# Optimization experiments

Hardware: AMD Instinct MI355X
Metric: run time of the kernel (lower is better)

The kernel has to match this reference:

```python
import jax, jax.numpy as jnp
import numpy as np

N = 50000      # nodes
E = 800000     # edges (avg degree 16)
D = 128        # in_channels == hidden_channels (required by x*M + x_hat*~M)
OUT = 64       # fc out_channels


def _linear_params(key, out_f, in_f):
    # torch.nn.Linear default init: U(-1/sqrt(in), 1/sqrt(in))
    bound = 1.0 / np.sqrt(in_f)
    kw, kb = jax.random.split(key)
    W = jax.random.uniform(kw, (out_f, in_f), jnp.float32, -bound, bound)
    b = jax.random.uniform(kb, (out_f,), jnp.float32, -bound, bound)
    return W, b


def setup_inputs() -> dict:
    key = jax.random.key(0)
    ks = jax.random.split(key, 8)
    x = jax.random.normal(ks[0], (N, D), jnp.float32)
    edge_index = jax.random.randint(ks[1], (2, E), 0, N, dtype=jnp.int64)
    edge_weight = jax.random.uniform(ks[2], (E,), jnp.float32)
    M = jax.random.randint(ks[3], (N, D), 0, 2) > 0  # bool mask
    W1, b1 = _linear_params(ks[4], D, D)
    W2, b2 = _linear_params(ks[5], D, D)
    W3, b3 = _linear_params(ks[6], D, D)
    Wf, bf = _linear_params(ks[7], OUT, D)
    # extra Parameter `bias` in each FPLayer is zero-initialized
    z = jnp.zeros((D,), jnp.float32)
    return {"edge_index": edge_index, "edge_weight": edge_weight, "x": x, "M": M,
            "W1": W1, "b1": b1, "bias1": z, "W2": W2, "b2": b2, "bias2": z,
            "W3": W3, "b3": b3, "bias3": z, "Wf": Wf, "bf": bf}


def reference(edge_index, edge_weight, x, M,
              W1, b1, bias1, W2, b2, bias2, W3, b3, bias3, Wf, bf):
    row, col = edge_index[0], edge_index[1]
    n = x.shape[0]
    # symmetric degree normalization based on destination-node in-degree
    deg = jax.ops.segment_sum(jnp.ones(row.shape[0], x.dtype), col, num_segments=n)
    safe = jnp.where(deg > 0, deg, 1.0)
    dinv = jnp.where(deg > 0, 1.0 / jnp.sqrt(safe), 0.0)
    norm = dinv[row] * dinv[col]  # [E]  (edge_weight is unused by message())

    def fp_layer(x_tilde, W, b, bias):
        msg = norm[:, None] * x_tilde[row]                      # [E, D] gather
        agg = jax.ops.segment_sum(msg, col, num_segments=n)     # [N, D] scatter-add
        return agg @ W.T + b + bias

    # conv1: x_hat = 0 -> x_tilde = x*M
    h = jax.nn.relu(fp_layer(jnp.where(M, x, 0.0), W1, b1, bias1))
    h = jax.nn.relu(fp_layer(jnp.where(M, x, h), W2, b2, bias2))
    h = jax.nn.relu(fp_layer(jnp.where(M, x, h), W3, b3, bias3))
    return h @ Wf.T + bf
```

## Files before the change

### kernel.cpp

```cpp
#include <hip/hip_runtime.h>

#define DD 128
#define OUTF 64
#define SCAP 128

typedef __attribute__((ext_vector_type(8))) _Float16 fp16x8;
typedef __attribute__((ext_vector_type(8))) unsigned short ushort8;
typedef __attribute__((ext_vector_type(4))) float floatx4;

union h16 { _Float16 f; unsigned short u; };

__global__ void probe_kernel(const unsigned char* m8, const int* ei32, int* flags) {
    __shared__ int s_u8, s_not64;
    int t = threadIdx.x;
    if (t == 0) { s_u8 = 0; s_not64 = 0; }
    __syncthreads();
    for (int i = t; i < 4096; i += 256)
        if ((i & 3) && m8[i]) s_u8 = 1;
    for (int i = t; i < 1024; i += 256)
        if (ei32[2 * i + 1]) s_not64 = 1;
    __syncthreads();
    if (t == 0) { flags[0] = s_u8; flags[1] = s_not64 ? 0 : 1; }
}

__global__ __launch_bounds__(256) void setup_kernel(
    const int* ei, const int* flags, int* cursor, int* __restrict__ slot, int E, int n,
    const float* __restrict__ x, const void* __restrict__ M,
    _Float16* __restrict__ xsel, int nd4,
    const float* __restrict__ W1, const float* __restrict__ W2,
    const float* __restrict__ W3, const float* __restrict__ Wf,
    _Float16* __restrict__ Bh1, _Float16* __restrict__ Bl1,
    _Float16* __restrict__ Bh2, _Float16* __restrict__ Bl2,
    _Float16* __restrict__ Bh3, _Float16* __restrict__ Bl3,
    _Float16* __restrict__ Bhf, _Float16* __restrict__ Blf,
    int nbSlot, int nbXt) {
    int bid = blockIdx.x;
    if (bid < nbSlot) {
        int e = bid * 256 + threadIdx.x;
        if (e >= E) return;
        int r, c;
        if (flags[1]) {
            const long long* p = (const long long*)ei;
            r = (int)p[e];
            c = (int)p[(size_t)E + e];
        } else {
            r = ei[e];
            c = ei[E + e];
        }
        r = min(max(r, 0), n - 1);
        c = min(max(c, 0), n - 1);
        int pos = atomicAdd(&cursor[c], 1);
        if (pos < SCAP)
            slot[(size_t)c * SCAP + pos] = r;
    } else if (bid < nbSlot + nbXt) {
        int i4 = (bid - nbSlot) * 256 + threadIdx.x;
        if (i4 >= nd4) return;
        size_t base = (size_t)i4 * 4;
        const float4 xv = *(const float4*)&x[base];
        int m0, m1, m2, m3;
        if (flags[0]) {
            const unsigned char* mp = (const unsigned char*)M + base;
            m0 = mp[0]; m1 = mp[1]; m2 = mp[2]; m3 = mp[3];
        } else {
            const int* mp = (const int*)M + base;
            m0 = mp[0]; m1 = mp[1]; m2 = mp[2]; m3 = mp[3];
        }
        h16 h0, h1, h2, h3;
        h0.f = (_Float16)xv.x; h1.f = (_Float16)xv.y;
        h2.f = (_Float16)xv.z; h3.f = (_Float16)xv.w;
        unsigned short s0 = m0 ? h0.u : (unsigned short)0xFFFF;
        unsigned short s1 = m1 ? h1.u : (unsigned short)0xFFFF;
        unsigned short s2 = m2 ? h2.u : (unsigned short)0xFFFF;
        unsigned short s3 = m3 ? h3.u : (unsigned short)0xFFFF;
        unsigned long long pk = (unsigned long long)s0 | ((unsigned long long)s1 << 16)
                              | ((unsigned long long)s2 << 32) | ((unsigned long long)s3 << 48);
        *(unsigned long long*)&xsel[base] = pk;
    } else {
        int tid = (bid - nbSlot - nbXt) * 256 + threadIdx.x;
        const float* W; _Float16 *Bh, *Bl; int NT, lt;
        if      (tid < 2048) { W = W1; Bh = Bh1; Bl = Bl1; NT = 8; lt = tid; }
        else if (tid < 4096) { W = W2; Bh = Bh2; Bl = Bl2; NT = 8; lt = tid - 2048; }
        else if (tid < 6144) { W = W3; Bh = Bh3; Bl = Bl3; NT = 8; lt = tid - 4096; }
        else if (tid < 7168) { W = Wf; Bh = Bhf; Bl = Blf; NT = 4; lt = tid - 6144; }
        else return;
        int lane = lt & 63;
        int g = lt >> 6;
        int nt = g % NT;
        int chunk = g / NT;
        int o = nt * 16 + (lane & 15);
        int k = chunk * 32 + (lane >> 4) * 8;
        const float* src = W + o * 128 + k;
#pragma unroll
        for (int j = 0; j < 8; j++) {
            float a = src[j];
            _Float16 h = (_Float16)a;
            Bh[(size_t)lt * 8 + j] = h;
            Bl[(size_t)lt * 8 + j] = (_Float16)(a - (float)h);
        }
    }
}

template <int MODE>
__global__ __launch_bounds__(256) void layer_kernel(
    const _Float16* __restrict__ xin,
    const int* __restrict__ cursor,
    const int* __restrict__ slot,
    const _Float16* __restrict__ Bh,
    const _Float16* __restrict__ Bl,
    const float* __restrict__ b,
    const float* __restrict__ bias,
    const _Float16* __restrict__ B2h,
    const _Float16* __restrict__ B2l,
    const float* __restrict__ b2,
    float* __restrict__ out_f,
    const _Float16* __restrict__ xsel,
    _Float16* __restrict__ xt_out,
    int n) {
    __shared__ __align__(16) _Float16 sh[4][16][136];
    int wid = (blockIdx.x * 256 + threadIdx.x) >> 6;
    int nwaves = n >> 4;
    if (wid >= nwaves) return;
    int n0 = wid * 16;
    int lane = threadIdx.x & 63;
    int li = lane & 15;
    int quad = lane >> 4;
    int wv = (threadIdx.x >> 6) & 3;

    for (int m = 0; m < 16; m++) {
        int node = n0 + m;
        int craw = cursor[node];
        int cnt = min(craw, SCAP);
        float dc = craw > 0 ? rsqrtf((float)craw) : 0.0f;
        const int* sl = slot + (size_t)node * SCAP;
        float acc[8] = {0.f, 0.f, 0.f, 0.f, 0.f, 0.f, 0.f, 0.f};
        for (int k = 0; k < cnt; k += 16) {
            int i0 = k + quad;
            int i1 = k + 4 + quad;
            int i2 = k + 8 + quad;
            int i3 = k + 12 + quad;
            int r0 = sl[min(i0, cnt - 1)];
            int r1 = sl[min(i1, cnt - 1)];
            int r2 = sl[min(i2, cnt - 1)];
            int r3 = sl[min(i3, cnt - 1)];
            int c0 = cursor[r0], c1 = cursor[r1], c2 = cursor[r2], c3 = cursor[r3];
            float w0 = (i0 < cnt && c0 > 0) ? dc * rsqrtf((float)c0) : 0.0f;
            float w1 = (i1 < cnt && c1 > 0) ? dc * rsqrtf((float)c1) : 0.0f;
            float w2 = (i2 < cnt && c2 > 0) ? dc * rsqrtf((float)c2) : 0.0f;
            float w3 = (i3 < cnt && c3 > 0) ? dc * rsqrtf((float)c3) : 0.0f;
            ushort8 u0 = *(const ushort8*)&xin[(size_t)r0 * DD + li * 8];
            ushort8 u1 = *(const ushort8*)&xin[(size_t)r1 * DD + li * 8];
            ushort8 u2 = *(const ushort8*)&xin[(size_t)r2 * DD + li * 8];
            ushort8 u3 = *(const ushort8*)&xin[(size_t)r3 * DD + li * 8];
#pragma unroll
            for (int j = 0; j < 8; j++) {
                h16 t0, t1, t2, t3;
                t0.u = (u0[j] == (unsigned short)0xFFFF) ? (unsigned short)0 : u0[j];
                t1.u = (u1[j] == (unsigned short)0xFFFF) ? (unsigned short)0 : u1[j];
                t2.u = (u2[j] == (unsigned short)0xFFFF) ? (unsigned short)0 : u2[j];
                t3.u = (u3[j] == (unsigned short)0xFFFF) ? (unsigned short)0 : u3[j];
                acc[j] += w0 * (float)t0.f + w1 * (float)t1.f
                        + w2 * (float)t2.f + w3 * (float)t3.f;
            }
        }
#pragma unroll
        for (int j = 0; j < 8; j++) {
            acc[j] += __shfl_xor(acc[j], 16);
            acc[j] += __shfl_xor(acc[j], 32);
        }
        if (quad == 0) {
            fp16x8 o;
#pragma unroll
            for (int j = 0; j < 8; j++) o[j] = (_Float16)acc[j];
            *(fp16x8*)&sh[wv][m][li * 8] = o;
        }
    }
    __asm__ volatile("s_waitcnt lgkmcnt(0)" ::: "memory");

    floatx4 acc[8];
#pragma unroll
    for (int nt = 0; nt < 8; nt++)
        acc[nt] = (floatx4){0.f, 0.f, 0.f, 0.f};
#pragma unroll
    for (int chunk = 0; chunk < 4; chunk++) {
        fp16x8 a = *(const fp16x8*)&sh[wv][li][chunk * 32 + quad * 8];
#pragma unroll
        for (int nt = 0; nt < 8; nt++) {
            size_t boff = (size_t)(((chunk * 8 + nt) << 6) + lane) * 8;
            fp16x8 b_h = *(const fp16x8*)&Bh[boff];
            fp16x8 b_l = *(const fp16x8*)&Bl[boff];
            acc[nt] = __builtin_amdgcn_mfma_f32_16x16x32_f16(a, b_h, acc[nt], 0, 0, 0);
            acc[nt] = __builtin_amdgcn_mfma_f32_16x16x32_f16(a, b_l, acc[nt], 0, 0, 0);
        }
    }
    __asm__ volatile("s_waitcnt lgkmcnt(0)" ::: "memory");

#pragma unroll
    for (int nt = 0; nt < 8; nt++) {
        int o = nt * 16 + li;
        float bb = b[o] + bias[o];
#pragma unroll
        for (int reg = 0; reg < 4; reg++) {
            float v = fmaxf(acc[nt][reg] + bb, 0.0f);
            sh[wv][quad * 4 + reg][o] = (_Float16)v;
        }
    }
    __asm__ volatile("s_waitcnt lgkmcnt(0)" ::: "memory");

    if (MODE == 0) {
#pragma unroll
        for (int it = 0; it < 4; it++) {
            int node = it * 4 + quad;
            size_t ix = (size_t)(n0 + node) * DD + li * 8;
            fp16x8 hv = *(const fp16x8*)&sh[wv][node][li * 8];
            fp16x8 xv = *(const fp16x8*)&xsel[ix];
            ushort8 xb = *(const ushort8*)&xsel[ix];
            fp16x8 o;
#pragma unroll
            for (int j = 0; j < 8; j++)
                o[j] = (xb[j] == (unsigned short)0xFFFF) ? hv[j] : xv[j];
            *(fp16x8*)&xt_out[ix] = o;
        }
    } else {
        floatx4 acc2[4];
#pragma unroll
        for (int nt = 0; nt < 4; nt++)
            acc2[nt] = (floatx4){0.f, 0.f, 0.f, 0.f};
#pragma unroll
        for (int chunk = 0; chunk < 4; chunk++) {
            fp16x8 a2 = *(const fp16x8*)&sh[wv][li][chunk * 32 + quad * 8];
#pragma unroll
            for (int nt = 0; nt < 4; nt++) {
                size_t boff = (size_t)(((chunk * 4 + nt) << 6) + lane) * 8;
                fp16x8 b_h = *(const fp16x8*)&B2h[boff];
                fp16x8 b_l = *(const fp16x8*)&B2l[boff];
                acc2[nt] = __builtin_amdgcn_mfma_f32_16x16x32_f16(a2, b_h, acc2[nt], 0, 0, 0);
                acc2[nt] = __builtin_amdgcn_mfma_f32_16x16x32_f16(a2, b_l, acc2[nt], 0, 0, 0);
            }
        }
        __asm__ volatile("s_waitcnt lgkmcnt(0)" ::: "memory");
        float* shf = (float*)&sh[wv][0][0];
#pragma unroll
        for (int nt = 0; nt < 4; nt++) {
            int o = nt * 16 + li;
            float bb = b2[o];
#pragma unroll
            for (int reg = 0; reg < 4; reg++)
                shf[(quad * 4 + reg) * 68 + o] = acc2[nt][reg] + bb;
        }
        __asm__ volatile("s_waitcnt lgkmcnt(0)" ::: "memory");
#pragma unroll
        for (int it = 0; it < 4; it++) {
            int node = it * 4 + quad;
            float4 v = *(const float4*)&shf[node * 68 + li * 4];
            *(float4*)&out_f[(size_t)(n0 + node) * OUTF + li * 4] = v;
        }
    }
}

extern "C" void kernel_launch(void* const* d_in, const int* in_sizes, int n_in,
                              void* d_out, int out_size, void* d_ws, size_t ws_size,
                              hipStream_t stream) {
    const int*   ei    = (const int*)d_in[0];
    const float* x     = (const float*)d_in[2];
    const void*  M     = d_in[3];
    const float* W1    = (const float*)d_in[4];
    const float* b1    = (const float*)d_in[5];
    const float* bias1 = (const float*)d_in[6];
    const float* W2    = (const float*)d_in[7];
    const float* b2    = (const float*)d_in[8];
    const float* bias2 = (const float*)d_in[9];
    const float* W3    = (const float*)d_in[10];
    const float* b3    = (const float*)d_in[11];
    const float* bias3 = (const float*)d_in[12];
    const float* Wf    = (const float*)d_in[13];
    const float* bf    = (const float*)d_in[14];

    const int E = in_sizes[1];
    const int N = in_sizes[2] / DD;
    const int ND = N * DD;

    char* w = (char*)d_ws;
    size_t off = 0;
    auto alloc = [&](size_t bytes) -> char* {
        char* p = w + off;
        off = (off + bytes + 255) & ~(size_t)255;
        return p;
    };
    int*   flags  = (int*)  alloc(32);
    int*   cursor = (int*)  alloc((size_t)N * 4);
    int*   slot   = (int*)  alloc((size_t)N * SCAP * 4);
    _Float16* xsel = (_Float16*)alloc((size_t)ND * 2);
    _Float16* xt   = (_Float16*)alloc((size_t)ND * 2);
    _Float16* Bh1 = (_Float16*)alloc(128 * 128 * 2);
    _Float16* Bl1 = (_Float16*)alloc(128 * 128 * 2);
    _Float16* Bh2 = (_Float16*)alloc(128 * 128 * 2);
    _Float16* Bl2 = (_Float16*)alloc(128 * 128 * 2);
    _Float16* Bh3 = (_Float16*)alloc(128 * 128 * 2);
    _Float16* Bl3 = (_Float16*)alloc(128 * 128 * 2);
    _Float16* Bhf = (_Float16*)alloc(64 * 128 * 2);
    _Float16* Blf = (_Float16*)alloc(64 * 128 * 2);
    (void)ws_size;

    const int nd4 = ND / 4;
    const int nbSlot = (E + 255) / 256;
    const int nbXt   = (nd4 + 255) / 256;
    const int nbPk   = 28;

    probe_kernel<<<1, 256, 0, stream>>>((const unsigned char*)M, ei, flags);
    hipMemsetAsync(cursor, 0, (size_t)N * 4, stream);
    setup_kernel<<<nbSlot + nbXt + nbPk, 256, 0, stream>>>(
        ei, flags, cursor, slot, E, N,
        x, M, xsel, nd4,
        W1, W2, W3, Wf,
        Bh1, Bl1, Bh2, Bl2, Bh3, Bl3, Bhf, Blf,
        nbSlot, nbXt);

    int nwaves = N / 16;
    int gGrid = (nwaves * 64 + 255) / 256;

    layer_kernel<0><<<gGrid, 256, 0, stream>>>(xsel, cursor, slot, Bh1, Bl1, b1, bias1,
                                               nullptr, nullptr, nullptr, nullptr,
                                               xsel, xt, N);
    layer_kernel<0><<<gGrid, 256, 0, stream>>>(xt, cursor, slot, Bh2, Bl2, b2, bias2,
                                               nullptr, nullptr, nullptr, nullptr,
                                               xsel, xt, N);
    layer_kernel<1><<<gGrid, 256, 0, stream>>>(xt, cursor, slot, Bh3, Bl3, b3, bias3,
                                               Bhf, Blf, bf, (float*)d_out,
                                               nullptr, nullptr, N);
}
```

Measured before the change: 346.8 us.

## Split fused gather-aggregate and MFMA GEMM into separate per-node agg and GEMM kernels

```diff
diff --git a/kernel.cpp b/kernel.cpp
--- a/kernel.cpp
+++ b/kernel.cpp
@@ -100,22 +100,80 @@
     }
 }
 
+template <int SENT>
+__global__ __launch_bounds__(256) void agg_kernel(const _Float16* __restrict__ xin,
+                                                  const int* __restrict__ cursor,
+                                                  const int* __restrict__ slot,
+                                                  _Float16* __restrict__ A, int n) {
+    int wave = (blockIdx.x * 256 + threadIdx.x) >> 6;
+    if (wave >= n) return;
+    int lane = threadIdx.x & 63;
+    int sid = lane >> 4;
+    int li = lane & 15;
+    int craw = cursor[wave];
+    int cnt = min(craw, SCAP);
+    float dc = craw > 0 ? rsqrtf((float)craw) : 0.0f;
+    const int* sl = slot + (size_t)wave * SCAP;
+    float acc[8] = {0.f, 0.f, 0.f, 0.f, 0.f, 0.f, 0.f, 0.f};
+    for (int k = 0; k < cnt; k += 16) {
+        int i0 = k + sid;
+        int i1 = k + 4 + sid;
+        int i2 = k + 8 + sid;
+        int i3 = k + 12 + sid;
+        int r0 = sl[min(i0, cnt - 1)];
+        int r1 = sl[min(i1, cnt - 1)];
+        int r2 = sl[min(i2, cnt - 1)];
+        int r3 = sl[min(i3, cnt - 1)];
+        int c0 = cursor[r0], c1 = cursor[r1], c2 = cursor[r2], c3 = cursor[r3];
+        float w0 = (i0 < cnt && c0 > 0) ? dc * rsqrtf((float)c0) : 0.0f;
+        float w1 = (i1 < cnt && c1 > 0) ? dc * rsqrtf((float)c1) : 0.0f;
+        float w2 = (i2 < cnt && c2 > 0) ? dc * rsqrtf((float)c2) : 0.0f;
+        float w3 = (i3 < cnt && c3 > 0) ? dc * rsqrtf((float)c3) : 0.0f;
+        ushort8 u0 = *(const ushort8*)&xin[(size_t)r0 * DD + li * 8];
+        ushort8 u1 = *(const ushort8*)&xin[(size_t)r1 * DD + li * 8];
+        ushort8 u2 = *(const ushort8*)&xin[(size_t)r2 * DD + li * 8];
+        ushort8 u3 = *(const ushort8*)&xin[(size_t)r3 * DD + li * 8];
+#pragma unroll
+        for (int j = 0; j < 8; j++) {
+            h16 t0, t1, t2, t3;
+            if (SENT) {
+                t0.u = (u0[j] == (unsigned short)0xFFFF) ? (unsigned short)0 : u0[j];
+                t1.u = (u1[j] == (unsigned short)0xFFFF) ? (unsigned short)0 : u1[j];
+                t2.u = (u2[j] == (unsigned short)0xFFFF) ? (unsigned short)0 : u2[j];
+                t3.u = (u3[j] == (unsigned short)0xFFFF) ? (unsigned short)0 : u3[j];
+            } else {
+                t0.u = u0[j]; t1.u = u1[j]; t2.u = u2[j]; t3.u = u3[j];
+            }
+            acc[j] += w0 * (float)t0.f + w1 * (float)t1.f
+                    + w2 * (float)t2.f + w3 * (float)t3.f;
+        }
+    }
+#pragma unroll
+    for (int j = 0; j < 8; j++) {
+        acc[j] += __shfl_xor(acc[j], 16);
+        acc[j] += __shfl_xor(acc[j], 32);
+    }
+    if (sid == 0) {
+        fp16x8 o;
+#pragma unroll
+        for (int j = 0; j < 8; j++) o[j] = (_Float16)acc[j];
+        *(fp16x8*)&A[(size_t)wave * DD + li * 8] = o;
+    }
+}
+
 template <int MODE>
-__global__ __launch_bounds__(256) void layer_kernel(
-    const _Float16* __restrict__ xin,
-    const int* __restrict__ cursor,
-    const int* __restrict__ slot,
-    const _Float16* __restrict__ Bh,
-    const _Float16* __restrict__ Bl,
-    const float* __restrict__ b,
-    const float* __restrict__ bias,
-    const _Float16* __restrict__ B2h,
-    const _Float16* __restrict__ B2l,
-    const float* __restrict__ b2,
-    float* __restrict__ out_f,
-    const _Float16* __restrict__ xsel,
-    _Float16* __restrict__ xt_out,
-    int n) {
+__global__ __launch_bounds__(256) void gemm_mfma(const _Float16* __restrict__ A,
+                                                 const _Float16* __restrict__ Bh,
+                                                 const _Float16* __restrict__ Bl,
+                                                 const float* __restrict__ b,
+                                                 const float* __restrict__ bias,
+                                                 const _Float16* __restrict__ B2h,
+                                                 const _Float16* __restrict__ B2l,
+                                                 const float* __restrict__ b2,
+                                                 float* __restrict__ out_f,
+                                                 const _Float16* __restrict__ xsel,
+                                                 _Float16* __restrict__ xt_out,
+                                                 int n) {
     __shared__ __align__(16) _Float16 sh[4][16][136];
     int wid = (blockIdx.x * 256 + threadIdx.x) >> 6;
     int nwaves = n >> 4;
@@ -126,63 +184,15 @@
     int quad = lane >> 4;
     int wv = (threadIdx.x >> 6) & 3;
 
-    for (int m = 0; m < 16; m++) {
-        int node = n0 + m;
-        int craw = cursor[node];
-        int cnt = min(craw, SCAP);
-        float dc = craw > 0 ? rsqrtf((float)craw) : 0.0f;
-        const int* sl = slot + (size_t)node * SCAP;
-        float acc[8] = {0.f, 0.f, 0.f, 0.f, 0.f, 0.f, 0.f, 0.f};
-        for (int k = 0; k < cnt; k += 16) {
-            int i0 = k + quad;
-            int i1 = k + 4 + quad;
-            int i2 = k + 8 + quad;
-            int i3 = k + 12 + quad;
-            int r0 = sl[min(i0, cnt - 1)];
-            int r1 = sl[min(i1, cnt - 1)];
-            int r2 = sl[min(i2, cnt - 1)];
-            int r3 = sl[min(i3, cnt - 1)];
-            int c0 = cursor[r0], c1 = cursor[r1], c2 = cursor[r2], c3 = cursor[r3];
-            float w0 = (i0 < cnt && c0 > 0) ? dc * rsqrtf((float)c0) : 0.0f;
-            float w1 = (i1 < cnt && c1 > 0) ? dc * rsqrtf((float)c1) : 0.0f;
-            float w2 = (i2 < cnt && c2 > 0) ? dc * rsqrtf((float)c2) : 0.0f;
-            float w3 = (i3 < cnt && c3 > 0) ? dc * rsqrtf((float)c3) : 0.0f;
-            ushort8 u0 = *(const ushort8*)&xin[(size_t)r0 * DD + li * 8];
-            ushort8 u1 = *(const ushort8*)&xin[(size_t)r1 * DD + li * 8];
-            ushort8 u2 = *(const ushort8*)&xin[(size_t)r2 * DD + li * 8];
-            ushort8 u3 = *(const ushort8*)&xin[(size_t)r3 * DD + li * 8];
-#pragma unroll
-            for (int j = 0; j < 8; j++) {
-                h16 t0, t1, t2, t3;
-                t0.u = (u0[j] == (unsigned short)0xFFFF) ? (unsigned short)0 : u0[j];
-                t1.u = (u1[j] == (unsigned short)0xFFFF) ? (unsigned short)0 : u1[j];
-                t2.u = (u2[j] == (unsigned short)0xFFFF) ? (unsigned short)0 : u2[j];
-                t3.u = (u3[j] == (unsigned short)0xFFFF) ? (unsigned short)0 : u3[j];
-                acc[j] += w0 * (float)t0.f + w1 * (float)t1.f
-                        + w2 * (float)t2.f + w3 * (float)t3.f;
-            }
-        }
-#pragma unroll
-        for (int j = 0; j < 8; j++) {
-            acc[j] += __shfl_xor(acc[j], 16);
-            acc[j] += __shfl_xor(acc[j], 32);
-        }
-        if (quad == 0) {
-            fp16x8 o;
-#pragma unroll
-            for (int j = 0; j < 8; j++) o[j] = (_Float16)acc[j];
-            *(fp16x8*)&sh[wv][m][li * 8] = o;
-        }
-    }
-    __asm__ volatile("s_waitcnt lgkmcnt(0)" ::: "memory");
-
     floatx4 acc[8];
 #pragma unroll
     for (int nt = 0; nt < 8; nt++)
         acc[nt] = (floatx4){0.f, 0.f, 0.f, 0.f};
+
+    const _Float16* arow = A + (size_t)(n0 + li) * DD + quad * 8;
 #pragma unroll
     for (int chunk = 0; chunk < 4; chunk++) {
-        fp16x8 a = *(const fp16x8*)&sh[wv][li][chunk * 32 + quad * 8];
+        fp16x8 a = *(const fp16x8*)(arow + chunk * 32);
 #pragma unroll
         for (int nt = 0; nt < 8; nt++) {
             size_t boff = (size_t)(((chunk * 8 + nt) << 6) + lane) * 8;
@@ -192,7 +202,6 @@
             acc[nt] = __builtin_amdgcn_mfma_f32_16x16x32_f16(a, b_l, acc[nt], 0, 0, 0);
         }
     }
-    __asm__ volatile("s_waitcnt lgkmcnt(0)" ::: "memory");
 
 #pragma unroll
     for (int nt = 0; nt < 8; nt++) {
@@ -291,6 +300,7 @@
     int*   slot   = (int*)  alloc((size_t)N * SCAP * 4);
     _Float16* xsel = (_Float16*)alloc((size_t)ND * 2);
     _Float16* xt   = (_Float16*)alloc((size_t)ND * 2);
+    _Float16* Aa   = (_Float16*)alloc((size_t)ND * 2);
     _Float16* Bh1 = (_Float16*)alloc(128 * 128 * 2);
     _Float16* Bl1 = (_Float16*)alloc(128 * 128 * 2);
     _Float16* Bh2 = (_Float16*)alloc(128 * 128 * 2);
@@ -317,14 +327,18 @@
 
     int nwaves = N / 16;
     int gGrid = (nwaves * 64 + 255) / 256;
-
-    layer_kernel<0><<<gGrid, 256, 0, stream>>>(xsel, cursor, slot, Bh1, Bl1, b1, bias1,
-                                               nullptr, nullptr, nullptr, nullptr,
-                                               xsel, xt, N);
-    layer_kernel<0><<<gGrid, 256, 0, stream>>>(xt, cursor, slot, Bh2, Bl2, b2, bias2,
-                                               nullptr, nullptr, nullptr, nullptr,
-                                               xsel, xt, N);
-    layer_kernel<1><<<gGrid, 256, 0, stream>>>(xt, cursor, slot, Bh3, Bl3, b3, bias3,
-                                               Bhf, Blf, bf, (float*)d_out,
-                                               nullptr, nullptr, N);
-}
+    int aggGrid = (N * 64 + 255) / 256;
+
+    agg_kernel<1><<<aggGrid, 256, 0, stream>>>(xsel, cursor, slot, Aa, N);
+    gemm_mfma<0><<<gGrid, 256, 0, stream>>>(Aa, Bh1, Bl1, b1, bias1,
+                                            nullptr, nullptr, nullptr, nullptr,
+                                            xsel, xt, N);
+    agg_kernel<0><<<aggGrid, 256, 0, stream>>>(xt, cursor, slot, Aa, N);
+    gemm_mfma<0><<<gGrid, 256, 0, stream>>>(Aa, Bh2, Bl2, b2, bias2,
+                                            nullptr, nullptr, nullptr, nullptr,
+                                            xsel, xt, N);
+    agg_kernel<0><<<aggGrid, 256, 0, stream>>>(xt, cursor, slot, Aa, N);
+    gemm_mfma<1><<<gGrid, 256, 0, stream>>>(Aa, Bh3, Bl3, b3, bias3,
+                                            Bhf, Blf, bf, (float*)d_out,
+                                            nullptr, nullptr, N);
+}
```

After: 306.1 us. -11.7%, faster.
